# Kernel tuning notes

Hardware: AMD Instinct MI355X
Metric: run time of the kernel (lower is better)

Reference implementation:

```python
import jax, jax.numpy as jnp
import numpy as np
import math

B, QLEN, KLEN = 8, 128, 1024
KDIM = QDIM = ADIM = ODIM = 512
HM, HC = 4, 4            # monotonic / chunkwise heads
CHUNK = 4                # chunkwise attention window
EPS = 1e-6
SHARPENING = 1.0
NEG_INF = float(np.finfo(np.float32).min)


def moving_sum(x, back, forward):
    """Windowed sum over last axis: out[k] = sum_{j=k-back}^{k+forward} x[j].
    Equivalent to the conv1d-with-ones-filter moving_sum in the torch code."""
    K = x.shape[-1]
    xp = jnp.pad(x, [(0, 0)] * (x.ndim - 1) + [(back, forward)])
    cs = jnp.cumsum(xp, axis=-1)
    L = back + forward + 1
    upper = jax.lax.slice_in_dim(cs, L - 1, L - 1 + K, axis=-1)
    lower = jnp.concatenate([jnp.zeros_like(cs[..., :1]),
                             jax.lax.slice_in_dim(cs, 0, K - 1, axis=-1)], axis=-1)
    return upper - lower


def safe_cumprod(x, eps):
    """exp(exclusive_cumsum(log(clip(x, eps, 1)))) along last axis."""
    logx = jnp.log(jnp.clip(x, eps, 1.0))
    excl = jnp.concatenate([jnp.zeros_like(logx[..., :1]),
                            jnp.cumsum(logx, axis=-1)[..., :-1]], axis=-1)
    return jnp.exp(excl)


def _heads(x, w, b, h):
    y = x @ w + b                                   # [B, L, ADIM]
    bs, L, _ = y.shape
    return y.reshape(bs, L, h, -1).transpose(0, 2, 1, 3)  # [B, h, L, d_k]


def setup_inputs() -> dict:
    key = jax.random.key(0)
    ks = jax.random.split(key, 16)
    s = 0.02
    f32 = jnp.float32
    return {
        "key_x": jax.random.normal(ks[0], (B, KLEN, KDIM), f32),
        "query_x": jax.random.normal(ks[1], (B, QLEN, QDIM), f32),
        "mask": jnp.ones((B, QLEN, KLEN), jnp.int32),
        "wk_m": jax.random.normal(ks[2], (KDIM, ADIM), f32) * s,
        "bk_m": jnp.zeros((ADIM,), f32),
        "wq_m": jax.random.normal(ks[3], (QDIM, ADIM), f32) * s,
        "bq_m": jnp.zeros((ADIM,), f32),
        "r": jnp.asarray(-4.0, f32),
        "wk_c": jax.random.normal(ks[4], (KDIM, ADIM), f32) * s,
        "bk_c": jnp.zeros((ADIM,), f32),
        "wq_c": jax.random.normal(ks[5], (QDIM, ADIM), f32) * s,
        "bq_c": jnp.zeros((ADIM,), f32),
        "wv": jax.random.normal(ks[6], (KDIM, ADIM), f32) * s,
        "bv": jnp.zeros((ADIM,), f32),
        "wo": jax.random.normal(ks[7], (ADIM, ODIM), f32) * s,
        "bo": jnp.zeros((ODIM,), f32),
    }


def reference(key_x, query_x, mask, wk_m, bk_m, wq_m, bq_m, r,
              wk_c, bk_c, wq_c, bq_c, wv, bv, wo, bo):
    scale = math.sqrt(ADIM)
    m = (mask[:, None] > 0)                                    # [B,1,Q,K]

    # ---- monotonic energy (scaled_dot + offset r) ----
    km = _heads(key_x, wk_m, bk_m, HM)                         # [B,HM,K,dk]
    qm = _heads(query_x, wq_m, bq_m, HM)                       # [B,HM,Q,dk]
    e_mono = jnp.einsum('bhqd,bhkd->bhqk', qm, km) / scale + r
    e_mono = jnp.where(m, e_mono, NEG_INF)

    # ---- monotonic alpha via safe_cumprod + per-step cumsum recurrence ----
    p_choose = jax.nn.sigmoid(e_mono)                          # [B,HM,Q,K]
    cp = safe_cumprod(1.0 - p_choose, EPS)                     # [B,HM,Q,K]
    aw0 = jnp.zeros((B, HM, KLEN), e_mono.dtype).at[..., 0].set(1.0)

    def step(aw_prev, pc):
        p_i, cp_i = pc                                         # [B,HM,K]
        aw = p_i * cp_i * jnp.cumsum(aw_prev / jnp.maximum(cp_i, EPS), axis=-1)
        return aw, aw

    _, alpha = jax.lax.scan(step, aw0,
                            (p_choose.transpose(2, 0, 1, 3),
                             cp.transpose(2, 0, 1, 3)))
    alpha = alpha.transpose(1, 2, 0, 3)                        # [B,HM,Q,K]

    # ---- chunkwise energy ----
    kc = _heads(key_x, wk_c, bk_c, HC)
    qc = _heads(query_x, wq_c, bq_c, HC)
    e_chunk = jnp.einsum('bhqd,bhkd->bhqk', qc, kc) / scale
    e_chunk = jnp.where(m, e_chunk, NEG_INF)

    # ---- efficient chunkwise attention (clipped-logit trick) ----
    e = e_chunk - jnp.max(e_chunk, axis=-1, keepdims=True)
    sexp = jnp.maximum(jnp.exp(e), 1e-5)[:, None]              # [B,1,HC,Q,K]
    denom = moving_sum(sexp, CHUNK - 1, 0)                     # [B,1,HC,Q,K]
    beta = sexp * moving_sum(alpha[:, :, None] * SHARPENING / denom,
                             0, CHUNK - 1)                     # [B,HM,HC,Q,K]
    beta = beta.reshape(B, HM * HC, QLEN, KLEN)

    # ---- context + output projection ----
    v = (key_x @ wv + bv).reshape(B, KLEN, HM * HC, ADIM // (HM * HC))
    cv = jnp.einsum('bhqk,bkhd->bqhd', beta, v).reshape(B, QLEN, ADIM)
    return cv @ wo + bo
```

## Files before the change

kernel.cpp:

```cpp
#include <hip/hip_runtime.h>
#include <hip/hip_bf16.h>


#define NEG_INF (-3.402823466e38f)
#define EPS_MOCHA 1e-6f
#define INV_SCALE 0.04419417382415922f

typedef _Float16 half8 __attribute__((ext_vector_type(8)));
typedef _Float16 half4v __attribute__((ext_vector_type(4)));
typedef float f32x4 __attribute__((ext_vector_type(4)));

#define ASTR 40

__device__ __forceinline__ float wave_incl_scan(float x)
{
    int v;
    v = __builtin_amdgcn_update_dpp(0, __builtin_bit_cast(int, x), 0x111, 0xF, 0xF, false);
    x += __builtin_bit_cast(float, v);
    v = __builtin_amdgcn_update_dpp(0, __builtin_bit_cast(int, x), 0x112, 0xF, 0xF, false);
    x += __builtin_bit_cast(float, v);
    v = __builtin_amdgcn_update_dpp(0, __builtin_bit_cast(int, x), 0x114, 0xF, 0xF, false);
    x += __builtin_bit_cast(float, v);
    v = __builtin_amdgcn_update_dpp(0, __builtin_bit_cast(int, x), 0x118, 0xF, 0xF, false);
    x += __builtin_bit_cast(float, v);
    v = __builtin_amdgcn_update_dpp(0, __builtin_bit_cast(int, x), 0x142, 0xA, 0xF, false);
    x += __builtin_bit_cast(float, v);
    v = __builtin_amdgcn_update_dpp(0, __builtin_bit_cast(int, x), 0x143, 0xC, 0xF, false);
    x += __builtin_bit_cast(float, v);
    return x;
}

__global__ __launch_bounds__(256) void prep_kernel(
    const float* __restrict__ key_x, const float* __restrict__ query_x,
    const float* __restrict__ wk_m, const float* __restrict__ wk_c,
    const float* __restrict__ wv, const float* __restrict__ wq_m,
    const float* __restrict__ wq_c, const float* __restrict__ wo,
    _Float16* __restrict__ K16, _Float16* __restrict__ Q16,
    _Float16* __restrict__ Wt5, _Float16* __restrict__ Wt_wo)
{
    __shared__ float T[64][65];
    const int bid = blockIdx.x;
    const int t = threadIdx.x;
    if (bid < 4608) {
        const float* in = (bid < 4096) ? key_x : query_x;
        _Float16* out = (bid < 4096) ? K16 : Q16;
        const size_t i = (size_t)(bid < 4096 ? bid : bid - 4096) * 256 + t;
        float4 v = *(const float4*)(in + i * 4);
        half4v h = {(_Float16)v.x, (_Float16)v.y, (_Float16)v.z, (_Float16)v.w};
        *(half4v*)(out + i * 4) = h;
        return;
    }
    const int idx = bid - 4608;
    const int z = idx >> 6, tile = idx & 63;
    const float* W = (z == 0) ? wk_m : (z == 1) ? wk_c : (z == 2) ? wv
                   : (z == 3) ? wq_m : (z == 4) ? wq_c : wo;
    _Float16* O = (z < 5) ? (Wt5 + (size_t)z * 262144) : Wt_wo;
    const int n0 = (tile & 7) * 64, k0 = (tile >> 3) * 64;
    const int rr = t >> 4, cc = (t & 15) * 4;
#pragma unroll
    for (int r = 0; r < 4; ++r) {
        int k = r * 16 + rr;
        float4 v = *(const float4*)(W + (size_t)(k0 + k) * 512 + n0 + cc);
        T[k][cc + 0] = v.x; T[k][cc + 1] = v.y;
        T[k][cc + 2] = v.z; T[k][cc + 3] = v.w;
    }
    __syncthreads();
    const int nn = t >> 2, kc = (t & 3) * 16;
    _Float16 tmp[16];
#pragma unroll
    for (int i = 0; i < 16; ++i) tmp[i] = (_Float16)T[kc + i][nn];
    _Float16* Op = O + (size_t)(n0 + nn) * 512 + k0 + kc;
    *(half8*)(Op)     = *(half8*)&tmp[0];
    *(half8*)(Op + 8) = *(half8*)&tmp[8];
}

__device__ __forceinline__ void mfma_step(half8 a[4], half8 b[4], f32x4 acc[4][4])
{
#pragma unroll
    for (int mt = 0; mt < 4; ++mt)
#pragma unroll
        for (int nt = 0; nt < 4; ++nt)
            acc[mt][nt] = __builtin_amdgcn_mfma_f32_16x16x32_f16(
                a[mt], b[nt], acc[mt][nt], 0, 0, 0);
}

__device__ __forceinline__ void gemm_core(
    const _Float16* __restrict__ A16, const _Float16* __restrict__ Wt,
    _Float16* As, _Float16* Bs, int m0, int n0,
    const float* __restrict__ bias, void* __restrict__ Cv, int f16o)
{
    const int tid = threadIdx.x;
    const int lane = tid & 63, wave = tid >> 6;
    const int wm = wave >> 1, wn = wave & 1;
    const int col = lane & 15, quad = lane >> 4;

    const int srow = tid >> 1, sseg = tid & 1;
    const _Float16* Ag = A16 + (size_t)(m0 + srow) * 512 + sseg * 16;
    const _Float16* Bg = Wt  + (size_t)(n0 + srow) * 512 + sseg * 16;
    _Float16* Al = As + srow * ASTR + sseg * 16;
    _Float16* Bl = Bs + srow * ASTR + sseg * 16;

    f32x4 acc[4][4];
#pragma unroll
    for (int mt = 0; mt < 4; ++mt)
#pragma unroll
        for (int nt = 0; nt < 4; ++nt) acc[mt][nt] = (f32x4)0.f;

    const _Float16* Afr = As + (size_t)(wm * 64 + col) * ASTR + quad * 8;
    const _Float16* Bfr = Bs + (size_t)(wn * 64 + col) * ASTR + quad * 8;

    half8 pa0, pa1, pb0, pb1;
    pa0 = *(const half8*)(Ag);
    pa1 = *(const half8*)(Ag + 8);
    pb0 = *(const half8*)(Bg);
    pb1 = *(const half8*)(Bg + 8);

    for (int ks = 0; ks < 16; ++ks) {
        __syncthreads();
        *(half8*)(Al)     = pa0;
        *(half8*)(Al + 8) = pa1;
        *(half8*)(Bl)     = pb0;
        *(half8*)(Bl + 8) = pb1;
        __syncthreads();
        if (ks + 1 < 16) {
            const int k0 = (ks + 1) * 32;
            pa0 = *(const half8*)(Ag + k0);
            pa1 = *(const half8*)(Ag + k0 + 8);
            pb0 = *(const half8*)(Bg + k0);
            pb1 = *(const half8*)(Bg + k0 + 8);
        }
        half8 a[4], b[4];
#pragma unroll
        for (int t = 0; t < 4; ++t) {
            a[t] = *(const half8*)(Afr + (size_t)t * 16 * ASTR);
            b[t] = *(const half8*)(Bfr + (size_t)t * 16 * ASTR);
        }
        mfma_step(a, b, acc);
    }

    float bnt[4];
#pragma unroll
    for (int nt = 0; nt < 4; ++nt)
        bnt[nt] = bias[n0 + wn * 64 + nt * 16 + col];
#pragma unroll
    for (int mt = 0; mt < 4; ++mt) {
        const int rowb = m0 + wm * 64 + mt * 16 + quad * 4;
#pragma unroll
        for (int nt = 0; nt < 4; ++nt) {
            const int cc = n0 + wn * 64 + nt * 16 + col;
#pragma unroll
            for (int r = 0; r < 4; ++r) {
                float v = acc[mt][nt][r] + bnt[nt];
                if (f16o)
                    ((_Float16*)Cv)[(size_t)(rowb + r) * 512 + cc] = (_Float16)v;
                else
                    ((float*)Cv)[(size_t)(rowb + r) * 512 + cc] = v;
            }
        }
    }
}

__global__ __launch_bounds__(256) void mfma_proj5(
    const _Float16* __restrict__ Akey, const _Float16* __restrict__ Aqry,
    const _Float16* __restrict__ Wt5,
    const float* __restrict__ b0, void* __restrict__ C0,
    const float* __restrict__ b1, void* __restrict__ C1,
    const float* __restrict__ b2, void* __restrict__ C2,
    const float* __restrict__ b3, void* __restrict__ C3,
    const float* __restrict__ b4, void* __restrict__ C4)
{
    __shared__ _Float16 As[128 * ASTR];
    __shared__ _Float16 Bs[128 * ASTR];
    const int g = blockIdx.y >> 2, nt128 = blockIdx.y & 3;
    const bool qry = g >= 3;
    if (qry && blockIdx.x >= 8) return;
    const _Float16* A16 = qry ? Aqry : Akey;
    const _Float16* Wt = Wt5 + (size_t)g * 262144;
    const float* bias = (g == 0) ? b0 : (g == 1) ? b1 : (g == 2) ? b2
                      : (g == 3) ? b3 : b4;
    void* Cv = (g == 0) ? C0 : (g == 1) ? C1 : (g == 2) ? C2
             : (g == 3) ? C3 : C4;
    const int f16o = (g == 2) ? 0 : 1;
    gemm_core(A16, Wt, As, Bs, blockIdx.x * 128, nt128 * 128, bias, Cv, f16o);
}

__global__ __launch_bounds__(256) void mfma_proj_out(
    const _Float16* __restrict__ A16, const _Float16* __restrict__ Wt,
    const float* __restrict__ bias, float* __restrict__ C)
{
    __shared__ _Float16 As[128 * ASTR];
    __shared__ _Float16 Bs[128 * ASTR];
    gemm_core(A16, Wt, As, Bs, blockIdx.x * 128, blockIdx.y * 128, bias, C, 0);
}

__device__ __forceinline__ void load_frags_g(
    const _Float16* Ap, const _Float16* Bp, int kk, half8 a[4], half8 b[4])
{
#pragma unroll
    for (int t = 0; t < 4; ++t) {
        a[t] = *(const half8*)(Ap + (size_t)t * 16 * 512 + kk);
        b[t] = *(const half8*)(Bp + (size_t)t * 16 * 512 + kk);
    }
}

__global__ __launch_bounds__(256) void energy_mfma(
    const _Float16* __restrict__ Qm, const _Float16* __restrict__ Km,
    const _Float16* __restrict__ Qc, const _Float16* __restrict__ Kc,
    const int* __restrict__ mask, float* __restrict__ e_mono,
    float* __restrict__ e_chunk, const float* __restrict__ r_ptr)
{
    const int tid = threadIdx.x;
    const int lane = tid & 63, wave = tid >> 6;
    const int wm = wave >> 1, wn = wave & 1;
    const int col = lane & 15, quad = lane >> 4;
    const int kt0 = blockIdx.x * 128;
    const int h = blockIdx.y;
    const int z = blockIdx.z;
    const int b = z & 7;
    const bool mono = z < 8;
    const _Float16* Qp = mono ? Qm : Qc;
    const _Float16* Kp = mono ? Km : Kc;
    float* out = mono ? e_mono : e_chunk;
    const float rv = mono ? r_ptr[0] : 0.f;

    const _Float16* Ap = Qp + (size_t)(b * 128 + wm * 64 + col) * 512 + h * 128 + quad * 8;
    const _Float16* Bp = Kp + (size_t)(b * 1024 + kt0 + wn * 64 + col) * 512 + h * 128 + quad * 8;

    f32x4 acc[4][4];
#pragma unroll
    for (int mt = 0; mt < 4; ++mt)
#pragma unroll
        for (int nt = 0; nt < 4; ++nt) acc[mt][nt] = (f32x4)0.f;

    half8 ab[3][4], bb[3][4];
    load_frags_g(Ap, Bp, 0, ab[0], bb[0]);
    load_frags_g(Ap, Bp, 32, ab[1], bb[1]);
#pragma unroll
    for (int ks = 0; ks < 4; ++ks) {
        const int cur = ks % 3, nxt = (ks + 2) % 3;
        if (ks + 2 < 4)
            load_frags_g(Ap, Bp, (ks + 2) * 32, ab[nxt], bb[nxt]);
        mfma_step(ab[cur], bb[cur], acc);
    }

#pragma unroll
    for (int mt = 0; mt < 4; ++mt) {
        const int qb = wm * 64 + mt * 16 + quad * 4;
#pragma unroll
        for (int nt = 0; nt < 4; ++nt) {
            const int kc = kt0 + wn * 64 + nt * 16 + col;
#pragma unroll
            for (int r = 0; r < 4; ++r) {
                const int q = qb + r;
                float v = acc[mt][nt][r] * INV_SCALE + rv;
                int mv = mask[((size_t)b * 128 + q) * 1024 + kc];
                out[(((size_t)b * 4 + h) * 128 + q) * 1024 + kc] = mv ? v : NEG_INF;
            }
        }
    }
}

__device__ __forceinline__ void transcend_row(
    const float* __restrict__ Erow, int lane, float o_pcp[16], float o_inv[16])
{
    const float* E = Erow + lane * 16;
    float e[16];
    *(float4*)&e[0]  = *(const float4*)(E);
    *(float4*)&e[4]  = *(const float4*)(E + 4);
    *(float4*)&e[8]  = *(const float4*)(E + 8);
    *(float4*)&e[12] = *(const float4*)(E + 12);

    float p[16], l[16];
#pragma unroll
    for (int i = 0; i < 16; ++i) {
        p[i] = 1.f / (1.f + expf(-e[i]));
        l[i] = logf(fmaxf(1.f - p[i], EPS_MOCHA));
    }
    float incl[16];
    incl[0] = l[0];
#pragma unroll
    for (int i = 1; i < 16; ++i) incl[i] = incl[i - 1] + l[i];
    float total = incl[15];
    float x = wave_incl_scan(total);
    float base = x - total;
#pragma unroll
    for (int i = 0; i < 16; ++i) {
        float cl = base + (i ? incl[i - 1] : 0.f);
        float cp = expf(cl);
        o_pcp[i] = p[i] * cp;
        o_inv[i] = 1.f / fmaxf(cp, EPS_MOCHA);
    }
}

__global__ __launch_bounds__(256) void alpha_pre(
    const float* __restrict__ e_mono, float* __restrict__ G,
    float* __restrict__ pcp)
{
    const int tid = threadIdx.x;
    const int lane = tid & 63;
    const int row = blockIdx.x * 4 + (tid >> 6);
    const int q = row & 127;

    float pq[16], iq[16];
    transcend_row(e_mono + (size_t)row * 1024, lane, pq, iq);

    float* P = pcp + (size_t)row * 1024 + lane * 16;
    *(float4*)(P)      = *(float4*)&pq[0];
    *(float4*)(P + 4)  = *(float4*)&pq[4];
    *(float4*)(P + 8)  = *(float4*)&pq[8];
    *(float4*)(P + 12) = *(float4*)&pq[12];

    float g[16];
    if (q == 0) {
#pragma unroll
        for (int i = 0; i < 16; ++i) g[i] = 0.f;
        if (lane == 0) g[0] = iq[0];
    } else {
        float pm[16], im[16];
        transcend_row(e_mono + (size_t)(row - 1) * 1024, lane, pm, im);
#pragma unroll
        for (int i = 0; i < 16; ++i) g[i] = pm[i] * iq[i];
    }
    float* Gp = G + (size_t)row * 1024 + lane * 16;
    *(float4*)(Gp)      = *(float4*)&g[0];
    *(float4*)(Gp + 4)  = *(float4*)&g[4];
    *(float4*)(Gp + 8)  = *(float4*)&g[8];
    *(float4*)(Gp + 12) = *(float4*)&g[12];
}

__global__ __launch_bounds__(64, 1) void alpha_scan(
    const float* __restrict__ G, float* __restrict__ S)
{
    const int lane = threadIdx.x;
    const int bh = blockIdx.x;
    const float* Gp = G + (size_t)bh * 131072 + lane * 16;
    float* Sp = S + (size_t)bh * 131072 + lane * 16;

    float bg[8][16];
#pragma unroll
    for (int s = 0; s < 8; ++s) {
        const float* Gq = Gp + (size_t)s * 1024;
        *(float4*)&bg[s][0]  = *(const float4*)(Gq);
        *(float4*)&bg[s][4]  = *(const float4*)(Gq + 4);
        *(float4*)&bg[s][8]  = *(const float4*)(Gq + 8);
        *(float4*)&bg[s][12] = *(const float4*)(Gq + 12);
    }

    float Sv[16];
#pragma unroll
    for (int i = 0; i < 16; ++i) Sv[i] = 1.f;

    for (int q8 = 0; q8 < 128; q8 += 8) {
#pragma unroll
        for (int s = 0; s < 8; ++s) {
            const int q = q8 + s;
            float g[16];
#pragma unroll
            for (int i = 0; i < 16; ++i) g[i] = bg[s][i];
            if (q + 8 < 128) {
                const float* Gq = Gp + (size_t)(q + 8) * 1024;
                *(float4*)&bg[s][0]  = *(const float4*)(Gq);
                *(float4*)&bg[s][4]  = *(const float4*)(Gq + 4);
                *(float4*)&bg[s][8]  = *(const float4*)(Gq + 8);
                *(float4*)&bg[s][12] = *(const float4*)(Gq + 12);
            }

            float incl[16];
            incl[0] = g[0] * Sv[0];
#pragma unroll
            for (int i = 1; i < 16; ++i)
                incl[i] = fmaf(g[i], Sv[i], incl[i - 1]);
            float total = incl[15];
            float x = wave_incl_scan(total);
            float base = x - total;
#pragma unroll
            for (int i = 0; i < 16; ++i) Sv[i] = base + incl[i];

            float* Sq = Sp + (size_t)q * 1024;
            *(float4*)(Sq)      = *(float4*)&Sv[0];
            *(float4*)(Sq + 4)  = *(float4*)&Sv[4];
            *(float4*)(Sq + 8)  = *(float4*)&Sv[8];
            *(float4*)(Sq + 12) = *(float4*)&Sv[12];
        }
    }
}

#define SW(k) ((k) + ((k) >> 3))

__global__ __launch_bounds__(256) void beta_kernel(
    const float* __restrict__ e_chunk, const float* __restrict__ pcp,
    const float* __restrict__ S, _Float16* __restrict__ beta)
{
    __shared__ float sm[SW(1023) + 1];
    __shared__ float tm[SW(1027) + 1];
    __shared__ float red[4];
    const int q = blockIdx.x, b = blockIdx.y;
    const int tid = threadIdx.x;
    const int lane = tid & 63, wid = tid >> 6;
    const int k4 = tid * 4;

    float av[4][4];
#pragma unroll
    for (int hm = 0; hm < 4; ++hm) {
        const size_t off = (((size_t)b * 4 + hm) * 128 + q) * 1024 + k4;
        float4 pv = *(const float4*)(pcp + off);
        float4 sv = *(const float4*)(S + off);
        av[hm][0] = pv.x * sv.x;
        av[hm][1] = pv.y * sv.y;
        av[hm][2] = pv.z * sv.z;
        av[hm][3] = pv.w * sv.w;
    }

    if (tid < 4) tm[SW(1024 + tid)] = 0.f;

    for (int hc = 0; hc < 4; ++hc) {
        float4 ev = *(const float4*)(e_chunk + (((size_t)b * 4 + hc) * 128 + q) * 1024 + k4);
        float e[4] = {ev.x, ev.y, ev.z, ev.w};

        float mx = fmaxf(fmaxf(e[0], e[1]), fmaxf(e[2], e[3]));
#pragma unroll
        for (int off = 32; off >= 1; off >>= 1)
            mx = fmaxf(mx, __shfl_xor(mx, off, 64));
        if (lane == 0) red[wid] = mx;
        __syncthreads();
        mx = fmaxf(fmaxf(red[0], red[1]), fmaxf(red[2], red[3]));

        float sx[4];
#pragma unroll
        for (int i = 0; i < 4; ++i) {
            sx[i] = fmaxf(expf(e[i] - mx), 1e-5f);
            sm[SW(k4 + i)] = sx[i];
        }
        __syncthreads();

        float den[4];
#pragma unroll
        for (int i = 0; i < 4; ++i) {
            int k = k4 + i;
            float d = sm[SW(k)];
            if (k >= 1) d += sm[SW(k - 1)];
            if (k >= 2) d += sm[SW(k - 2)];
            if (k >= 3) d += sm[SW(k - 3)];
            den[i] = d;
        }

#pragma unroll
        for (int hm = 0; hm < 4; ++hm) {
            float t[4] = {av[hm][0] / den[0], av[hm][1] / den[1],
                          av[hm][2] / den[2], av[hm][3] / den[3]};
#pragma unroll
            for (int i = 0; i < 4; ++i) tm[SW(k4 + i)] = t[i];
            __syncthreads();
            float o[4];
#pragma unroll
            for (int i = 0; i < 4; ++i) {
                int k = k4 + i;
                float ms = tm[SW(k)] + tm[SW(k + 1)] + tm[SW(k + 2)] + tm[SW(k + 3)];
                o[i] = sx[i] * ms;
            }
            _Float16* Brow = beta + (((size_t)b * 16 + hm * 4 + hc) * 128 + q) * 1024;
            half4v hv = {(_Float16)o[0], (_Float16)o[1], (_Float16)o[2], (_Float16)o[3]};
            *(half4v*)(Brow + k4) = hv;
            __syncthreads();
        }
    }
}

__global__ __launch_bounds__(256) void context_kernel(
    const _Float16* __restrict__ beta, const float* __restrict__ V,
    _Float16* __restrict__ cv16)
{
    __shared__ float bS[32][64];
    __shared__ float vS[32][32];
    const int qh = blockIdx.x, h = blockIdx.y, b = blockIdx.z;
    const int tid = threadIdx.x;
    const int ty = tid >> 3, tx = tid & 7;
    const int q0 = qh * 64;

    const _Float16* Bbase = beta + (((size_t)b * 16 + h) * 128 + q0) * 1024;
    const float* Vbase = V + (size_t)b * 1024 * 512 + h * 32;

    float acc[2][4];
#pragma unroll
    for (int i = 0; i < 2; ++i)
#pragma unroll
        for (int j = 0; j < 4; ++j) acc[i][j] = 0.f;

    for (int k0 = 0; k0 < 1024; k0 += 32) {
        {
            int r = tid >> 2, c = tid & 3;
            half8 v = *(const half8*)(Bbase + (size_t)r * 1024 + k0 + c * 8);
#pragma unroll
            for (int j = 0; j < 8; ++j) bS[c * 8 + j][r] = (float)v[j];
        }
        {
            int kk = tid >> 3, c = tid & 7;
            float4 v = *(const float4*)(Vbase + (size_t)(k0 + kk) * 512 + c * 4);
            *(float4*)&vS[kk][c * 4] = v;
        }
        __syncthreads();
#pragma unroll
        for (int kk = 0; kk < 32; ++kk) {
            float a0 = bS[kk][ty * 2], a1 = bS[kk][ty * 2 + 1];
            float bb[4];
            *(float4*)bb = *(const float4*)&vS[kk][tx * 4];
#pragma unroll
            for (int j = 0; j < 4; ++j) {
                acc[0][j] = fmaf(a0, bb[j], acc[0][j]);
                acc[1][j] = fmaf(a1, bb[j], acc[1][j]);
            }
        }
        __syncthreads();
    }
#pragma unroll
    for (int i = 0; i < 2; ++i) {
        _Float16* Cp = cv16 + ((size_t)b * 128 + q0 + ty * 2 + i) * 512 + h * 32 + tx * 4;
        half4v hv = {(_Float16)acc[i][0], (_Float16)acc[i][1],
                     (_Float16)acc[i][2], (_Float16)acc[i][3]};
        *(half4v*)Cp = hv;
    }
}

extern "C" void kernel_launch(void* const* d_in, const int* in_sizes, int n_in,
                              void* d_out, int out_size, void* d_ws, size_t ws_size,
                              hipStream_t stream)
{
    const float* key_x   = (const float*)d_in[0];
    const float* query_x = (const float*)d_in[1];
    const int*   mask    = (const int*)d_in[2];
    const float* wk_m = (const float*)d_in[3];
    const float* bk_m = (const float*)d_in[4];
    const float* wq_m = (const float*)d_in[5];
    const float* bq_m = (const float*)d_in[6];
    const float* r    = (const float*)d_in[7];
    const float* wk_c = (const float*)d_in[8];
    const float* bk_c = (const float*)d_in[9];
    const float* wq_c = (const float*)d_in[10];
    const float* bq_c = (const float*)d_in[11];
    const float* wv   = (const float*)d_in[12];
    const float* bv   = (const float*)d_in[13];
    const float* wo   = (const float*)d_in[14];
    const float* bo   = (const float*)d_in[15];
    float* out = (float*)d_out;

    float* ws = (float*)d_ws;
    _Float16* hws = (_Float16*)d_ws;
    const size_t MEGF = 1024 * 1024;
    _Float16* K16   = hws;
    _Float16* Q16   = hws + 8 * MEGF;
    _Float16* Wt5   = hws + 9 * MEGF;
    _Float16* Km16  = hws + 12 * MEGF;
    _Float16* Kc16  = hws + 16 * MEGF;
    _Float16* Qm16  = hws + 20 * MEGF;
    _Float16* Qc16  = hws + 20 * MEGF + MEGF / 2;
    float* e_mono  = ws + 11 * MEGF;
    float* e_chunk = ws + 15 * MEGF;
    float* V       = ws + 19 * MEGF;
    float* G       = ws;
    float* pcp     = ws + 8 * MEGF;
    float* S       = ws + 23 * MEGF;
    _Float16* beta16 = hws;
    _Float16* Wt_wo = hws + 55 * MEGF;
    _Float16* cv16  = hws + 55 * MEGF + MEGF / 2;

    prep_kernel<<<dim3(4992), 256, 0, stream>>>(
        key_x, query_x, wk_m, wk_c, wv, wq_m, wq_c, wo,
        K16, Q16, Wt5, Wt_wo);
    mfma_proj5<<<dim3(64, 20), 256, 0, stream>>>(
        K16, Q16, Wt5,
        bk_m, Km16, bk_c, Kc16, bv, V, bq_m, Qm16, bq_c, Qc16);
    energy_mfma<<<dim3(8, 4, 16), 256, 0, stream>>>(
        Qm16, Km16, Qc16, Kc16, mask, e_mono, e_chunk, r);
    alpha_pre<<<dim3(1024), 256, 0, stream>>>(e_mono, G, pcp);
    alpha_scan<<<dim3(32), 64, 0, stream>>>(G, S);
    beta_kernel<<<dim3(128, 8), 256, 0, stream>>>(e_chunk, pcp, S, beta16);
    context_kernel<<<dim3(2, 16, 8), 256, 0, stream>>>(beta16, V, cv16);
    mfma_proj_out<<<dim3(8, 4), 256, 0, stream>>>(cv16, Wt_wo, bo, out);
}
```

Before: 272.1 us.

## Stage GEMM tiles via global_load_lds and store chunk energies as fp16

Replaces the register-prefetch-then-store LDS staging in the projection GEMMs with direct global-to-LDS loads (global_load_lds), using an unpadded 32-wide LDS layout. The energy kernel now uses the same LDS-staged GEMM path instead of loading MFMA fragments straight from global memory. Chunk energies are written and read as fp16 rather than fp32, halving that intermediate's traffic. The trade-offs are fewer registers but less overlap, since the register prefetch of the next tile is gone. The unpadded LDS layout may cause bank conflicts, and fp16 energies lose precision before the exp.

```diff
diff --git a/kernel.cpp b/kernel.cpp
--- a/kernel.cpp
+++ b/kernel.cpp
@@ -9,8 +9,6 @@
 typedef _Float16 half8 __attribute__((ext_vector_type(8)));
 typedef _Float16 half4v __attribute__((ext_vector_type(4)));
 typedef float f32x4 __attribute__((ext_vector_type(4)));
-
-#define ASTR 40
 
 __device__ __forceinline__ float wave_incl_scan(float x)
 {
@@ -84,60 +82,62 @@
                 a[mt], b[nt], acc[mt][nt], 0, 0, 0);
 }
 
-__device__ __forceinline__ void gemm_core(
-    const _Float16* __restrict__ A16, const _Float16* __restrict__ Wt,
-    _Float16* As, _Float16* Bs, int m0, int n0,
-    const float* __restrict__ bias, void* __restrict__ Cv, int f16o)
+__device__ __forceinline__ void stage16(const _Float16* src, _Float16* dst)
+{
+    __builtin_amdgcn_global_load_lds(
+        (const __attribute__((address_space(1))) void*)src,
+        (__attribute__((address_space(3))) void*)dst, 16, 0, 0);
+}
+
+template <int NSTEPS>
+__device__ __forceinline__ void gemm_acc(
+    const _Float16* __restrict__ Abase, const _Float16* __restrict__ Bbase,
+    _Float16* As, _Float16* Bs, f32x4 acc[4][4])
 {
     const int tid = threadIdx.x;
     const int lane = tid & 63, wave = tid >> 6;
     const int wm = wave >> 1, wn = wave & 1;
     const int col = lane & 15, quad = lane >> 4;
-
-    const int srow = tid >> 1, sseg = tid & 1;
-    const _Float16* Ag = A16 + (size_t)(m0 + srow) * 512 + sseg * 16;
-    const _Float16* Bg = Wt  + (size_t)(n0 + srow) * 512 + sseg * 16;
-    _Float16* Al = As + srow * ASTR + sseg * 16;
-    _Float16* Bl = Bs + srow * ASTR + sseg * 16;
-
-    f32x4 acc[4][4];
-#pragma unroll
-    for (int mt = 0; mt < 4; ++mt)
-#pragma unroll
-        for (int nt = 0; nt < 4; ++nt) acc[mt][nt] = (f32x4)0.f;
-
-    const _Float16* Afr = As + (size_t)(wm * 64 + col) * ASTR + quad * 8;
-    const _Float16* Bfr = Bs + (size_t)(wn * 64 + col) * ASTR + quad * 8;
-
-    half8 pa0, pa1, pb0, pb1;
-    pa0 = *(const half8*)(Ag);
-    pa1 = *(const half8*)(Ag + 8);
-    pb0 = *(const half8*)(Bg);
-    pb1 = *(const half8*)(Bg + 8);
-
-    for (int ks = 0; ks < 16; ++ks) {
+    const int r0 = tid >> 2, seg = tid & 3;
+
+    const _Float16* Ag0 = Abase + (size_t)r0 * 512 + seg * 8;
+    const _Float16* Ag1 = Ag0 + (size_t)64 * 512;
+    const _Float16* Bg0 = Bbase + (size_t)r0 * 512 + seg * 8;
+    const _Float16* Bg1 = Bg0 + (size_t)64 * 512;
+    _Float16* Ad0 = As + tid * 8;
+    _Float16* Ad1 = As + 2048 + tid * 8;
+    _Float16* Bd0 = Bs + tid * 8;
+    _Float16* Bd1 = Bs + 2048 + tid * 8;
+
+    const _Float16* Afr = As + (size_t)(wm * 64 + col) * 32 + quad * 8;
+    const _Float16* Bfr = Bs + (size_t)(wn * 64 + col) * 32 + quad * 8;
+
+#pragma unroll
+    for (int ks = 0; ks < NSTEPS; ++ks) {
         __syncthreads();
-        *(half8*)(Al)     = pa0;
-        *(half8*)(Al + 8) = pa1;
-        *(half8*)(Bl)     = pb0;
-        *(half8*)(Bl + 8) = pb1;
+        stage16(Ag0 + ks * 32, Ad0);
+        stage16(Ag1 + ks * 32, Ad1);
+        stage16(Bg0 + ks * 32, Bd0);
+        stage16(Bg1 + ks * 32, Bd1);
         __syncthreads();
-        if (ks + 1 < 16) {
-            const int k0 = (ks + 1) * 32;
-            pa0 = *(const half8*)(Ag + k0);
-            pa1 = *(const half8*)(Ag + k0 + 8);
-            pb0 = *(const half8*)(Bg + k0);
-            pb1 = *(const half8*)(Bg + k0 + 8);
-        }
         half8 a[4], b[4];
 #pragma unroll
         for (int t = 0; t < 4; ++t) {
-            a[t] = *(const half8*)(Afr + (size_t)t * 16 * ASTR);
-            b[t] = *(const half8*)(Bfr + (size_t)t * 16 * ASTR);
+            a[t] = *(const half8*)(Afr + (size_t)t * 16 * 32);
+            b[t] = *(const half8*)(Bfr + (size_t)t * 16 * 32);
         }
         mfma_step(a, b, acc);
     }
-
+}
+
+__device__ __forceinline__ void proj_epilogue(
+    f32x4 acc[4][4], const float* __restrict__ bias, void* __restrict__ Cv,
+    int m0, int n0, int f16o)
+{
+    const int tid = threadIdx.x;
+    const int lane = tid & 63, wave = tid >> 6;
+    const int wm = wave >> 1, wn = wave & 1;
+    const int col = lane & 15, quad = lane >> 4;
     float bnt[4];
 #pragma unroll
     for (int nt = 0; nt < 4; ++nt)
@@ -169,8 +169,8 @@
     const float* __restrict__ b3, void* __restrict__ C3,
     const float* __restrict__ b4, void* __restrict__ C4)
 {
-    __shared__ _Float16 As[128 * ASTR];
-    __shared__ _Float16 Bs[128 * ASTR];
+    __shared__ _Float16 As[4096];
+    __shared__ _Float16 Bs[4096];
     const int g = blockIdx.y >> 2, nt128 = blockIdx.y & 3;
     const bool qry = g >= 3;
     if (qry && blockIdx.x >= 8) return;
@@ -181,34 +181,41 @@
     void* Cv = (g == 0) ? C0 : (g == 1) ? C1 : (g == 2) ? C2
              : (g == 3) ? C3 : C4;
     const int f16o = (g == 2) ? 0 : 1;
-    gemm_core(A16, Wt, As, Bs, blockIdx.x * 128, nt128 * 128, bias, Cv, f16o);
+    const int m0 = blockIdx.x * 128, n0 = nt128 * 128;
+
+    f32x4 acc[4][4];
+#pragma unroll
+    for (int mt = 0; mt < 4; ++mt)
+#pragma unroll
+        for (int nt = 0; nt < 4; ++nt) acc[mt][nt] = (f32x4)0.f;
+    gemm_acc<16>(A16 + (size_t)m0 * 512, Wt + (size_t)n0 * 512, As, Bs, acc);
+    proj_epilogue(acc, bias, Cv, m0, n0, f16o);
 }
 
 __global__ __launch_bounds__(256) void mfma_proj_out(
     const _Float16* __restrict__ A16, const _Float16* __restrict__ Wt,
     const float* __restrict__ bias, float* __restrict__ C)
 {
-    __shared__ _Float16 As[128 * ASTR];
-    __shared__ _Float16 Bs[128 * ASTR];
-    gemm_core(A16, Wt, As, Bs, blockIdx.x * 128, blockIdx.y * 128, bias, C, 0);
-}
-
-__device__ __forceinline__ void load_frags_g(
-    const _Float16* Ap, const _Float16* Bp, int kk, half8 a[4], half8 b[4])
-{
-#pragma unroll
-    for (int t = 0; t < 4; ++t) {
-        a[t] = *(const half8*)(Ap + (size_t)t * 16 * 512 + kk);
-        b[t] = *(const half8*)(Bp + (size_t)t * 16 * 512 + kk);
-    }
+    __shared__ _Float16 As[4096];
+    __shared__ _Float16 Bs[4096];
+    const int m0 = blockIdx.x * 128, n0 = blockIdx.y * 128;
+    f32x4 acc[4][4];
+#pragma unroll
+    for (int mt = 0; mt < 4; ++mt)
+#pragma unroll
+        for (int nt = 0; nt < 4; ++nt) acc[mt][nt] = (f32x4)0.f;
+    gemm_acc<16>(A16 + (size_t)m0 * 512, Wt + (size_t)n0 * 512, As, Bs, acc);
+    proj_epilogue(acc, bias, C, m0, n0, 0);
 }
 
 __global__ __launch_bounds__(256) void energy_mfma(
     const _Float16* __restrict__ Qm, const _Float16* __restrict__ Km,
     const _Float16* __restrict__ Qc, const _Float16* __restrict__ Kc,
     const int* __restrict__ mask, float* __restrict__ e_mono,
-    float* __restrict__ e_chunk, const float* __restrict__ r_ptr)
-{
+    _Float16* __restrict__ e_chunk16, const float* __restrict__ r_ptr)
+{
+    __shared__ _Float16 As[4096];
+    __shared__ _Float16 Bs[4096];
     const int tid = threadIdx.x;
     const int lane = tid & 63, wave = tid >> 6;
     const int wm = wave >> 1, wn = wave & 1;
@@ -220,28 +227,15 @@
     const bool mono = z < 8;
     const _Float16* Qp = mono ? Qm : Qc;
     const _Float16* Kp = mono ? Km : Kc;
-    float* out = mono ? e_mono : e_chunk;
     const float rv = mono ? r_ptr[0] : 0.f;
 
-    const _Float16* Ap = Qp + (size_t)(b * 128 + wm * 64 + col) * 512 + h * 128 + quad * 8;
-    const _Float16* Bp = Kp + (size_t)(b * 1024 + kt0 + wn * 64 + col) * 512 + h * 128 + quad * 8;
-
     f32x4 acc[4][4];
 #pragma unroll
     for (int mt = 0; mt < 4; ++mt)
 #pragma unroll
         for (int nt = 0; nt < 4; ++nt) acc[mt][nt] = (f32x4)0.f;
-
-    half8 ab[3][4], bb[3][4];
-    load_frags_g(Ap, Bp, 0, ab[0], bb[0]);
-    load_frags_g(Ap, Bp, 32, ab[1], bb[1]);
-#pragma unroll
-    for (int ks = 0; ks < 4; ++ks) {
-        const int cur = ks % 3, nxt = (ks + 2) % 3;
-        if (ks + 2 < 4)
-            load_frags_g(Ap, Bp, (ks + 2) * 32, ab[nxt], bb[nxt]);
-        mfma_step(ab[cur], bb[cur], acc);
-    }
+    gemm_acc<4>(Qp + (size_t)(b * 128) * 512 + h * 128,
+                Kp + (size_t)(b * 1024 + kt0) * 512 + h * 128, As, Bs, acc);
 
 #pragma unroll
     for (int mt = 0; mt < 4; ++mt) {
@@ -254,7 +248,10 @@
                 const int q = qb + r;
                 float v = acc[mt][nt][r] * INV_SCALE + rv;
                 int mv = mask[((size_t)b * 128 + q) * 1024 + kc];
-                out[(((size_t)b * 4 + h) * 128 + q) * 1024 + kc] = mv ? v : NEG_INF;
+                v = mv ? v : NEG_INF;
+                const size_t oi = (((size_t)b * 4 + h) * 128 + q) * 1024 + kc;
+                if (mono) e_mono[oi] = v;
+                else      e_chunk16[oi] = (_Float16)v;
             }
         }
     }
@@ -388,7 +385,7 @@
 #define SW(k) ((k) + ((k) >> 3))
 
 __global__ __launch_bounds__(256) void beta_kernel(
-    const float* __restrict__ e_chunk, const float* __restrict__ pcp,
+    const _Float16* __restrict__ e_chunk16, const float* __restrict__ pcp,
     const float* __restrict__ S, _Float16* __restrict__ beta)
 {
     __shared__ float sm[SW(1023) + 1];
@@ -414,8 +411,8 @@
     if (tid < 4) tm[SW(1024 + tid)] = 0.f;
 
     for (int hc = 0; hc < 4; ++hc) {
-        float4 ev = *(const float4*)(e_chunk + (((size_t)b * 4 + hc) * 128 + q) * 1024 + k4);
-        float e[4] = {ev.x, ev.y, ev.z, ev.w};
+        half4v ev = *(const half4v*)(e_chunk16 + (((size_t)b * 4 + hc) * 128 + q) * 1024 + k4);
+        float e[4] = {(float)ev[0], (float)ev[1], (float)ev[2], (float)ev[3]};
 
         float mx = fmaxf(fmaxf(e[0], e[1]), fmaxf(e[2], e[3]));
 #pragma unroll
@@ -554,7 +551,7 @@
     _Float16* Qm16  = hws + 20 * MEGF;
     _Float16* Qc16  = hws + 20 * MEGF + MEGF / 2;
     float* e_mono  = ws + 11 * MEGF;
-    float* e_chunk = ws + 15 * MEGF;
+    _Float16* e_chunk16 = hws + 30 * MEGF;
     float* V       = ws + 19 * MEGF;
     float* G       = ws;
     float* pcp     = ws + 8 * MEGF;
@@ -570,10 +567,10 @@
         K16, Q16, Wt5,
         bk_m, Km16, bk_c, Kc16, bv, V, bq_m, Qm16, bq_c, Qc16);
     energy_mfma<<<dim3(8, 4, 16), 256, 0, stream>>>(
-        Qm16, Km16, Qc16, Kc16, mask, e_mono, e_chunk, r);
+        Qm16, Km16, Qc16, Kc16, mask, e_mono, e_chunk16, r);
     alpha_pre<<<dim3(1024), 256, 0, stream>>>(e_mono, G, pcp);
     alpha_scan<<<dim3(32), 64, 0, stream>>>(G, S);
-    beta_kernel<<<dim3(128, 8), 256, 0, stream>>>(e_chunk, pcp, S, beta16);
+    beta_kernel<<<dim3(128, 8), 256, 0, stream>>>(e_chunk16, pcp, S, beta16);
     context_kernel<<<dim3(2, 16, 8), 256, 0, stream>>>(beta16, V, cv16);
     mfma_proj_out<<<dim3(8, 4), 256, 0, stream>>>(cv16, Wt_wo, bo, out);
 }
```

Result: no change. 274.1 us (+0.7%).
